# Kernel tuning notes

Hardware: AMD Instinct MI355X
Metric: run time of the kernel (lower is better)

## Reference

```python
import jax, jax.numpy as jnp
import numpy as np

B, S, D, H = 4, 1024, 768, 12
Dh = D // H
EPS = 1e-5


def _layer_norm(x, g, b):
    mu = jnp.mean(x, axis=-1, keepdims=True)
    var = jnp.var(x, axis=-1, keepdims=True)
    return (x - mu) * jax.lax.rsqrt(var + EPS) * g + b


def _mha(q_in, k_in, v_in, Wq, Wk, Wv, Wo, bias):
    # Wq/Wk/Wv: [H, D, Dh] (per-head projections, batched over heads)
    q = jnp.einsum('bsd,hdk->bhsk', q_in, Wq)
    k = jnp.einsum('btd,hdk->bhtk', k_in, Wk)
    v = jnp.einsum('btd,hdk->bhtk', v_in, Wv)
    w = jnp.einsum('bhsk,bhtk->bhst', q, k) * (Dh ** -0.5)
    a = jax.nn.softmax(w + bias, axis=-1)  # bias: 0 / -inf additive mask
    o = jnp.einsum('bhst,bhtk->bhsk', a, v)
    o = o.transpose(0, 2, 1, 3).reshape(q_in.shape[0], q_in.shape[1], H * Dh)  # concat heads
    return o @ Wo


def setup_inputs():
    key = jax.random.key(0)
    ks = jax.random.split(key, 16)
    s = 0.02
    inp = {
        'key_enc': jax.random.normal(ks[0], (B, S, D), jnp.float32),
        'value_enc': jax.random.normal(ks[1], (B, S, D), jnp.float32),
        'x': jax.random.normal(ks[2], (B, S, D), jnp.float32),
        'src_mask': jnp.ones((B, S), jnp.int32),
        'tgt_mask': jnp.ones((B, S), jnp.int32),
        'Wq_m': jax.random.normal(ks[3], (H, D, Dh), jnp.float32) * s,
        'Wk_m': jax.random.normal(ks[4], (H, D, Dh), jnp.float32) * s,
        'Wv_m': jax.random.normal(ks[5], (H, D, Dh), jnp.float32) * s,
        'Wo_m': jax.random.normal(ks[6], (D, D), jnp.float32) * s,
        'Wq_c': jax.random.normal(ks[7], (H, D, Dh), jnp.float32) * s,
        'Wk_c': jax.random.normal(ks[8], (H, D, Dh), jnp.float32) * s,
        'Wv_c': jax.random.normal(ks[9], (H, D, Dh), jnp.float32) * s,
        'Wo_c': jax.random.normal(ks[10], (D, D), jnp.float32) * s,
        'ln1_g': jnp.ones((D,), jnp.float32), 'ln1_b': jnp.zeros((D,), jnp.float32),
        'ln2_g': jnp.ones((D,), jnp.float32), 'ln2_b': jnp.zeros((D,), jnp.float32),
        'ln3_g': jnp.ones((D,), jnp.float32), 'ln3_b': jnp.zeros((D,), jnp.float32),
        'W1': jax.random.normal(ks[11], (D, 4 * D), jnp.float32) * s,
        'b1': jnp.zeros((4 * D,), jnp.float32),
        'W2': jax.random.normal(ks[12], (4 * D, D), jnp.float32) * s,
        'b2': jnp.zeros((D,), jnp.float32),
    }
    return inp


def reference(key_enc, value_enc, x, src_mask, tgt_mask,
              Wq_m, Wk_m, Wv_m, Wo_m, Wq_c, Wk_c, Wv_c, Wo_c,
              ln1_g, ln1_b, ln2_g, ln2_b, ln3_g, ln3_b, W1, b1, W2, b2):
    neg_inf = jnp.float32(-jnp.inf)
    causal = jnp.tril(jnp.ones((S, S), bool))
    # masked self-attn: causal AND target padding mask (mask broadcasts over query rows)
    allow_m = causal[None, None, :, :] & (tgt_mask[:, None, None, :] != 0)
    bias_m = jnp.where(allow_m, jnp.float32(0.0), neg_inf)
    h = _layer_norm(x + _mha(x, x, x, Wq_m, Wk_m, Wv_m, Wo_m, bias_m), ln1_g, ln1_b)
    # cross-attn: keys from `key_enc`, values from `value_enc`, queries from decoder stream
    allow_c = (src_mask[:, None, None, :] != 0)
    bias_c = jnp.where(allow_c, jnp.float32(0.0), neg_inf)
    h = _layer_norm(h + _mha(h, key_enc, value_enc, Wq_c, Wk_c, Wv_c, Wo_c, bias_c), ln2_g, ln2_b)
    # MLP with exact (erf) GELU, as torch nn.GELU default
    mlp = jax.nn.gelu(h @ W1 + b1, approximate=False) @ W2 + b2
    return _layer_norm(h + mlp, ln3_g, ln3_b)
```

## Files before the change

### kernel.cpp

```cpp
#include <hip/hip_runtime.h>
#include <math.h>

#define BB 4
#define SS 1024
#define DD 768
#define HH 12
#define DHD 64
#define MROWS 4096
#define FF 3072
#define WPC (DD * DD)
#define NSPLITROWS 24576

typedef unsigned short u16;
typedef float f32x4 __attribute__((ext_vector_type(4)));
typedef __bf16 bf16x8 __attribute__((ext_vector_type(8)));
typedef unsigned short u16x8 __attribute__((ext_vector_type(8)));
typedef unsigned short u16x4 __attribute__((ext_vector_type(4)));

static __device__ __forceinline__ float bf2f(u16 u) {
    union { unsigned int i; float f; } c; c.i = ((unsigned int)u) << 16; return c.f;
}
static __device__ __forceinline__ u16 f2bf(float f) {
    return __builtin_bit_cast(u16, static_cast<__bf16>(f));
}
static __device__ __forceinline__ int xcd_swz(int total) {
    const int bid = (int)blockIdx.x;
    return (bid & 7) * (total >> 3) + (bid >> 3);
}

#define LDST 40

static __device__ __forceinline__ void gemm128_core(
    const u16* __restrict__ A, const u16* __restrict__ Bt,
    int K,
    const float* __restrict__ bias, int do_gelu,
    u16* __restrict__ Cbf, int ldcbf, int cboff,
    int row0, int col0, u16* As, u16* Bs)
{
    const int tid  = threadIdx.x;
    const int lane = tid & 63;
    const int w    = tid >> 6;
    const int wm = (w >> 1) * 64;
    const int wn = (w & 1) * 64;

    const int srow = tid >> 1;
    const int skc  = (tid & 1) * 16;

    const u16* Ap = A  + (size_t)(row0 + srow) * K + skc;
    const u16* Bp = Bt + (size_t)(col0 + srow) * K + skc;
    u16* AsW = &As[srow * LDST + skc];
    u16* BsW = &Bs[srow * LDST + skc];

    const int fr = lane & 15;
    const int fk = (lane >> 4) * 8;

    f32x4 acc[4][4] = {};

    u16x8 aa0, aa1, ba0, ba1;
    u16x8 ab0, ab1, bb0, bb1;
    aa0 = *(const u16x8*)(Ap);
    aa1 = *(const u16x8*)(Ap + 8);
    ba0 = *(const u16x8*)(Bp);
    ba1 = *(const u16x8*)(Bp + 8);
    ab0 = *(const u16x8*)(Ap + 32);
    ab1 = *(const u16x8*)(Ap + 40);
    bb0 = *(const u16x8*)(Bp + 32);
    bb1 = *(const u16x8*)(Bp + 40);

    for (int k0 = 0; k0 < K; k0 += 64) {
        if (k0) __syncthreads();
        *(u16x8*)(AsW)     = aa0;
        *(u16x8*)(AsW + 8) = aa1;
        *(u16x8*)(BsW)     = ba0;
        *(u16x8*)(BsW + 8) = ba1;
        __syncthreads();
        if (k0 + 64 < K) {
            aa0 = *(const u16x8*)(Ap + k0 + 64);
            aa1 = *(const u16x8*)(Ap + k0 + 72);
            ba0 = *(const u16x8*)(Bp + k0 + 64);
            ba1 = *(const u16x8*)(Bp + k0 + 72);
        }
        {
            bf16x8 af[4], bfv[4];
#pragma unroll
            for (int mi = 0; mi < 4; ++mi)
                af[mi] = __builtin_bit_cast(bf16x8,
                    *(const u16x8*)(&As[(wm + 16 * mi + fr) * LDST + fk]));
#pragma unroll
            for (int ni = 0; ni < 4; ++ni)
                bfv[ni] = __builtin_bit_cast(bf16x8,
                    *(const u16x8*)(&Bs[(wn + 16 * ni + fr) * LDST + fk]));
#pragma unroll
            for (int mi = 0; mi < 4; ++mi)
#pragma unroll
                for (int ni = 0; ni < 4; ++ni)
                    acc[mi][ni] = __builtin_amdgcn_mfma_f32_16x16x32_bf16(
                        af[mi], bfv[ni], acc[mi][ni], 0, 0, 0);
        }

        __syncthreads();
        *(u16x8*)(AsW)     = ab0;
        *(u16x8*)(AsW + 8) = ab1;
        *(u16x8*)(BsW)     = bb0;
        *(u16x8*)(BsW + 8) = bb1;
        __syncthreads();
        if (k0 + 96 < K) {
            ab0 = *(const u16x8*)(Ap + k0 + 96);
            ab1 = *(const u16x8*)(Ap + k0 + 104);
            bb0 = *(const u16x8*)(Bp + k0 + 96);
            bb1 = *(const u16x8*)(Bp + k0 + 104);
        }
        {
            bf16x8 af[4], bfv[4];
#pragma unroll
            for (int mi = 0; mi < 4; ++mi)
                af[mi] = __builtin_bit_cast(bf16x8,
                    *(const u16x8*)(&As[(wm + 16 * mi + fr) * LDST + fk]));
#pragma unroll
            for (int ni = 0; ni < 4; ++ni)
                bfv[ni] = __builtin_bit_cast(bf16x8,
                    *(const u16x8*)(&Bs[(wn + 16 * ni + fr) * LDST + fk]));
#pragma unroll
            for (int mi = 0; mi < 4; ++mi)
#pragma unroll
                for (int ni = 0; ni < 4; ++ni)
                    acc[mi][ni] = __builtin_amdgcn_mfma_f32_16x16x32_bf16(
                        af[mi], bfv[ni], acc[mi][ni], 0, 0, 0);
        }
    }

    const int orow0 = row0 + wm + (lane >> 4) * 4;
    const int ocol0 = col0 + wn + fr;
#pragma unroll
    for (int mi = 0; mi < 4; ++mi) {
#pragma unroll
        for (int ni = 0; ni < 4; ++ni) {
            const int col = ocol0 + ni * 16;
            const float bv = bias ? bias[col] : 0.0f;
#pragma unroll
            for (int r = 0; r < 4; ++r) {
                const int row = orow0 + mi * 16 + r;
                float v = acc[mi][ni][r] + bv;
                if (do_gelu) v = 0.5f * v * (1.0f + erff(v * 0.70710678118654752f));
                Cbf[(size_t)row * ldcbf + cboff + col] = f2bf(v);
            }
        }
    }
}

__global__ __launch_bounds__(256) void gemm128_mlp1(
    const u16* __restrict__ A, const u16* __restrict__ Bt,
    const float* __restrict__ bias, u16* __restrict__ Cbf)
{
    __shared__ u16 As[128 * LDST];
    __shared__ u16 Bs[128 * LDST];
    const int lid = xcd_swz(24 * 32);
    gemm128_core(A, Bt, DD, bias, 1, Cbf, FF, 0,
                 (lid / 24) * 128, (lid % 24) * 128, As, Bs);
}

__global__ __launch_bounds__(256) void gemm128_proj(
    const u16* __restrict__ BFx, const u16* __restrict__ BFK,
    const u16* __restrict__ BFV, const u16* __restrict__ Wm6,
    u16* __restrict__ QKV, u16* __restrict__ KVc)
{
    __shared__ u16 As[128 * LDST];
    __shared__ u16 Bs[128 * LDST];
    const int fid = xcd_swz(960);
    const u16* A; const u16* B; u16* C; int ldc, coff, row0, col0;
    if (fid < 576) {
        A = BFx; B = Wm6; C = QKV; ldc = 3 * DD; coff = 0;
        row0 = (fid / 18) * 128; col0 = (fid % 18) * 128;
    } else if (fid < 768) {
        const int l = fid - 576;
        A = BFK; B = Wm6 + 4 * WPC; C = KVc; ldc = 2 * DD; coff = 0;
        row0 = (l / 6) * 128; col0 = (l % 6) * 128;
    } else {
        const int l = fid - 768;
        A = BFV; B = Wm6 + 5 * WPC; C = KVc; ldc = 2 * DD; coff = DD;
        row0 = (l / 6) * 128; col0 = (l % 6) * 128;
    }
    gemm128_core(A, B, DD, nullptr, 0, C, ldc, coff, row0, col0, As, Bs);
}

static __device__ __forceinline__ void gemm64_core(
    const u16* __restrict__ A, const u16* __restrict__ Bt,
    int N, int Kstride, int Klen,
    const float* __restrict__ bias,
    const float* __restrict__ residf, const u16* __restrict__ residb,
    u16* __restrict__ Cbf, int ldcbf, int cboff,
    int row0, int col0, u16* As, u16* Bs)
{
    const int tid  = threadIdx.x;
    const int lane = tid & 63;
    const int w    = tid >> 6;
    const int wm = (w >> 1) * 32;
    const int wn = (w & 1) * 64;

    const int arow = tid >> 2;
    const int akc  = (tid & 3) * 8;
    const int brow = tid >> 1;
    const int bkc  = (tid & 1) * 16;

    const u16* Ap = A  + (size_t)(row0 + arow) * Kstride + akc;
    const u16* Bp = Bt + (size_t)(col0 + brow) * Kstride + bkc;
    u16* AsW = &As[arow * LDST + akc];
    u16* BsW = &Bs[brow * LDST + bkc];

    const int fr = lane & 15;
    const int fk = (lane >> 4) * 8;

    f32x4 acc[2][4] = {};

    u16x8 a0, b00, b01, a1, b10, b11;
    a0  = *(const u16x8*)(Ap);
    b00 = *(const u16x8*)(Bp);
    b01 = *(const u16x8*)(Bp + 8);
    a1  = *(const u16x8*)(Ap + 32);
    b10 = *(const u16x8*)(Bp + 32);
    b11 = *(const u16x8*)(Bp + 40);

    for (int k0 = 0; k0 < Klen; k0 += 64) {
        if (k0) __syncthreads();
        *(u16x8*)AsW       = a0;
        *(u16x8*)BsW       = b00;
        *(u16x8*)(BsW + 8) = b01;
        __syncthreads();
        if (k0 + 64 < Klen) {
            a0  = *(const u16x8*)(Ap + k0 + 64);
            b00 = *(const u16x8*)(Bp + k0 + 64);
            b01 = *(const u16x8*)(Bp + k0 + 72);
        }
        {
            bf16x8 af[2], bfv[4];
#pragma unroll
            for (int mi = 0; mi < 2; ++mi)
                af[mi] = __builtin_bit_cast(bf16x8,
                    *(const u16x8*)(&As[(wm + 16 * mi + fr) * LDST + fk]));
#pragma unroll
            for (int ni = 0; ni < 4; ++ni)
                bfv[ni] = __builtin_bit_cast(bf16x8,
                    *(const u16x8*)(&Bs[(wn + 16 * ni + fr) * LDST + fk]));
#pragma unroll
            for (int mi = 0; mi < 2; ++mi)
#pragma unroll
                for (int ni = 0; ni < 4; ++ni)
                    acc[mi][ni] = __builtin_amdgcn_mfma_f32_16x16x32_bf16(
                        af[mi], bfv[ni], acc[mi][ni], 0, 0, 0);
        }

        __syncthreads();
        *(u16x8*)AsW       = a1;
        *(u16x8*)BsW       = b10;
        *(u16x8*)(BsW + 8) = b11;
        __syncthreads();
        if (k0 + 96 < Klen) {
            a1  = *(const u16x8*)(Ap + k0 + 96);
            b10 = *(const u16x8*)(Bp + k0 + 96);
            b11 = *(const u16x8*)(Bp + k0 + 104);
        }
        {
            bf16x8 af[2], bfv[4];
#pragma unroll
            for (int mi = 0; mi < 2; ++mi)
                af[mi] = __builtin_bit_cast(bf16x8,
                    *(const u16x8*)(&As[(wm + 16 * mi + fr) * LDST + fk]));
#pragma unroll
            for (int ni = 0; ni < 4; ++ni)
                bfv[ni] = __builtin_bit_cast(bf16x8,
                    *(const u16x8*)(&Bs[(wn + 16 * ni + fr) * LDST + fk]));
#pragma unroll
            for (int mi = 0; mi < 2; ++mi)
#pragma unroll
                for (int ni = 0; ni < 4; ++ni)
                    acc[mi][ni] = __builtin_amdgcn_mfma_f32_16x16x32_bf16(
                        af[mi], bfv[ni], acc[mi][ni], 0, 0, 0);
        }
    }

    const int orow0 = row0 + wm + (lane >> 4) * 4;
    const int ocol0 = col0 + wn + fr;
#pragma unroll
    for (int mi = 0; mi < 2; ++mi) {
#pragma unroll
        for (int ni = 0; ni < 4; ++ni) {
            const int col = ocol0 + ni * 16;
            const float bv = bias ? bias[col] : 0.0f;
#pragma unroll
            for (int r = 0; r < 4; ++r) {
                const int row = orow0 + mi * 16 + r;
                float v = acc[mi][ni][r] + bv;
                if (residf) v += residf[(size_t)row * N + col];
                if (residb) v += bf2f(residb[(size_t)row * N + col]);
                Cbf[(size_t)row * ldcbf + cboff + col] = f2bf(v);
            }
        }
    }
}

__global__ __launch_bounds__(256) void gemm64(
    const u16* __restrict__ A, const u16* __restrict__ Bt, int K,
    const float* __restrict__ residf, const u16* __restrict__ residb,
    u16* __restrict__ Cbf, int ldcbf)
{
    __shared__ u16 As[64 * LDST];
    __shared__ u16 Bs[128 * LDST];
    const int lid = xcd_swz(6 * 64);
    gemm64_core(A, Bt, DD, K, K, nullptr, residf, residb, Cbf, ldcbf, 0,
                (lid / 6) * 64, (lid % 6) * 128, As, Bs);
}

__global__ __launch_bounds__(256) void gemm64_sk(
    const u16* __restrict__ A, const u16* __restrict__ Bt,
    u16* __restrict__ Cpair)
{
    __shared__ u16 As[64 * LDST];
    __shared__ u16 Bs[128 * LDST];
    const int lid = xcd_swz(6 * 64 * 2);
    const int x = lid % 6;
    const int rem = lid / 6;
    const int y = rem % 64;
    const int z = rem / 64;
    const int koff = z * (FF / 2);
    gemm64_core(A + koff, Bt + koff, DD, FF, FF / 2,
                nullptr, nullptr, nullptr,
                Cpair + (size_t)z * MROWS * DD, DD, 0,
                y * 64, x * 128, As, Bs);
}

static __device__ __forceinline__ void tcvt_body(
    const float* __restrict__ in, u16* __restrict__ out,
    int K, int N, int bx, int by)
{
    __shared__ float t[32][33];
    const int n0 = bx * 32, k0 = by * 32;
    const int tx = threadIdx.x & 31, ty = threadIdx.x >> 5;
#pragma unroll
    for (int j = 0; j < 4; ++j)
        t[ty + j * 8][tx] = in[(size_t)(k0 + ty + j * 8) * N + n0 + tx];
    __syncthreads();
#pragma unroll
    for (int j = 0; j < 4; ++j)
        out[(size_t)(n0 + ty + j * 8) * K + k0 + tx] = f2bf(t[tx][ty + j * 8]);
}

__global__ __launch_bounds__(256) void prep_all(
    const float* __restrict__ x, const float* __restrict__ key_enc,
    const float* __restrict__ value_enc,
    u16* __restrict__ BFx, u16* __restrict__ BFK, u16* __restrict__ BFV,
    const float* __restrict__ wq_m, const float* __restrict__ wk_m,
    const float* __restrict__ wv_m, const float* __restrict__ wq_c,
    const float* __restrict__ wk_c, const float* __restrict__ wv_c,
    u16* __restrict__ Wm6,
    const float* __restrict__ wom, const float* __restrict__ woc,
    const float* __restrict__ w1, const float* __restrict__ w2,
    u16* __restrict__ womt, u16* __restrict__ woct,
    u16* __restrict__ w1t, u16* __restrict__ w2t)
{
    const int fid = (int)blockIdx.x;
    const int tid = threadIdx.x;
    if (fid < 9216) {
        const int z = fid / 3072;
        const float* s = (z == 0) ? x : (z == 1) ? key_enc : value_enc;
        u16* d = (z == 0) ? BFx : (z == 1) ? BFK : BFV;
        const int i = (fid % 3072) * 256 + tid;
        float4 v = ((const float4*)s)[i];
        ushort4 o;
        o.x = f2bf(v.x); o.y = f2bf(v.y); o.z = f2bf(v.z); o.w = f2bf(v.w);
        ((ushort4*)d)[i] = o;
    } else if (fid < 12672) {
        const int l = fid - 9216;
        const int z = l / 48;
        const int r = l % 48;
        const int wi = z / 12, head = z % 12;
        const float* wsel = (wi == 0) ? wq_m : (wi == 1) ? wk_m :
                            (wi == 2) ? wv_m : (wi == 3) ? wq_c :
                            (wi == 4) ? wk_c : wv_c;
        const float* ib = wsel + (size_t)head * DD * DHD;
        u16* ob = Wm6 + (size_t)wi * WPC + (size_t)head * DHD * DD;
        __shared__ float t[32][33];
        const int n0 = (r % 2) * 32, k0 = (r / 2) * 32;
        const int tx = tid & 31, ty = tid >> 5;
#pragma unroll
        for (int j = 0; j < 4; ++j)
            t[ty + j * 8][tx] = ib[(size_t)(k0 + ty + j * 8) * DHD + n0 + tx];
        __syncthreads();
#pragma unroll
        for (int j = 0; j < 4; ++j)
            ob[(size_t)(n0 + ty + j * 8) * DD + k0 + tx] = f2bf(t[tx][ty + j * 8]);
    } else {
        const int l = fid - 12672;
        if (l < 576) {
            tcvt_body(wom, womt, DD, DD, l % 24, l / 24);
        } else if (l < 1152) {
            const int m = l - 576;
            tcvt_body(woc, woct, DD, DD, m % 24, m / 24);
        } else if (l < 3456) {
            const int m = l - 1152;
            tcvt_body(w1, w1t, DD, FF, m % 96, m / 96);
        } else {
            const int m = l - 3456;
            tcvt_body(w2, w2t, FF, DD, m % 24, m / 24);
        }
    }
}

#define KAST 72
#define PAST 136
#define CSC 0.18033688011112042f

__global__ __launch_bounds__(256) void attn_cross_kernel(
    const u16* __restrict__ Q, int ldq,
    const u16* __restrict__ K, const u16* __restrict__ V, int ldkv,
    const int* __restrict__ kmask, u16* __restrict__ O)
{
    const int lid = xcd_swz(16 * BB * HH);
    const int qt = lid % 16;
    const int bh = lid / 16;
    const int b  = bh / HH;
    const int h  = bh % HH;
    const int tid  = threadIdx.x;
    const int lane = tid & 63;
    const int w    = tid >> 6;
    const int lr = lane & 15;
    const int lg = lane >> 4;

    __shared__ u16 Ks[128 * KAST];
    __shared__ u16 Ps[64 * PAST];
    __shared__ u16 Vt[64 * PAST];

    const int q0w = qt * 64 + w * 16;

    bf16x8 qf[2];
    {
        const u16* qp = Q + (size_t)(b * SS + q0w + lr) * ldq + h * DHD + lg * 8;
        qf[0] = __builtin_bit_cast(bf16x8, *(const u16x8*)(qp));
        qf[1] = __builtin_bit_cast(bf16x8, *(const u16x8*)(qp + 32));
    }

    const int sr  = tid >> 1;
    const int scb = (tid & 1) * 32;
    const int vk  = tid >> 1;
    const int vdb = (tid & 1) * 32;
    const int k6  = vk & 63;
    const int vcol = ((vk >> 6) << 6) | ((k6 & 15) << 2) | (k6 >> 4);

    f32x4 acc[4] = {};
    float lsum[4] = {0.0f, 0.0f, 0.0f, 0.0f};

    u16x8 kr0, kr1, kr2, kr3, vr0, vr1, vr2, vr3;
    {
        const u16* kp = K + (size_t)(b * SS + sr) * ldkv + h * DHD + scb;
        kr0 = *(const u16x8*)(kp);
        kr1 = *(const u16x8*)(kp + 8);
        kr2 = *(const u16x8*)(kp + 16);
        kr3 = *(const u16x8*)(kp + 24);
        const u16* vp = V + (size_t)(b * SS + vk) * ldkv + h * DHD + vdb;
        vr0 = *(const u16x8*)(vp);
        vr1 = *(const u16x8*)(vp + 8);
        vr2 = *(const u16x8*)(vp + 16);
        vr3 = *(const u16x8*)(vp + 24);
    }

    for (int kt = 0; kt < 8; ++kt) {
        const int kcol0 = kt * 128;
        if (kt) __syncthreads();

        *(u16x8*)(&Ks[sr * KAST + scb])      = kr0;
        *(u16x8*)(&Ks[sr * KAST + scb + 8])  = kr1;
        *(u16x8*)(&Ks[sr * KAST + scb + 16]) = kr2;
        *(u16x8*)(&Ks[sr * KAST + scb + 24]) = kr3;
#pragma unroll
        for (int j = 0; j < 8; ++j) Vt[(vdb + j) * PAST + vcol]      = vr0[j];
#pragma unroll
        for (int j = 0; j < 8; ++j) Vt[(vdb + 8 + j) * PAST + vcol]  = vr1[j];
#pragma unroll
        for (int j = 0; j < 8; ++j) Vt[(vdb + 16 + j) * PAST + vcol] = vr2[j];
#pragma unroll
        for (int j = 0; j < 8; ++j) Vt[(vdb + 24 + j) * PAST + vcol] = vr3[j];
        __syncthreads();

        if (kt + 1 < 8) {
            const int kn = kcol0 + 128;
            const u16* kp = K + (size_t)(b * SS + kn + sr) * ldkv + h * DHD + scb;
            kr0 = *(const u16x8*)(kp);
            kr1 = *(const u16x8*)(kp + 8);
            kr2 = *(const u16x8*)(kp + 16);
            kr3 = *(const u16x8*)(kp + 24);
            const u16* vp = V + (size_t)(b * SS + kn + vk) * ldkv + h * DHD + vdb;
            vr0 = *(const u16x8*)(vp);
            vr1 = *(const u16x8*)(vp + 8);
            vr2 = *(const u16x8*)(vp + 16);
            vr3 = *(const u16x8*)(vp + 24);
        }

        f32x4 s[8] = {};
#pragma unroll
        for (int fi = 0; fi < 8; ++fi) {
            bf16x8 kf0 = __builtin_bit_cast(bf16x8, *(const u16x8*)(&Ks[(fi * 16 + lr) * KAST + lg * 8]));
            bf16x8 kf1 = __builtin_bit_cast(bf16x8, *(const u16x8*)(&Ks[(fi * 16 + lr) * KAST + 32 + lg * 8]));
            s[fi] = __builtin_amdgcn_mfma_f32_16x16x32_bf16(qf[0], kf0, s[fi], 0, 0, 0);
            s[fi] = __builtin_amdgcn_mfma_f32_16x16x32_bf16(qf[1], kf1, s[fi], 0, 0, 0);
        }

        float biasf[8];
#pragma unroll
        for (int fi = 0; fi < 8; ++fi)
            biasf[fi] = kmask[b * SS + kcol0 + fi * 16 + lr] ? 0.0f : -INFINITY;

#pragma unroll
        for (int r = 0; r < 4; ++r) {
            const int prow = (w * 16 + lg * 4 + r) * PAST;
            u16x4 pk0, pk1;
            float rs = 0.0f;
#pragma unroll
            for (int fi = 0; fi < 8; ++fi) {
                const float v = fmaf(s[fi][r], CSC, biasf[fi]);
                const float pv = exp2f(v);
                if (fi < 4) pk0[fi] = f2bf(pv); else pk1[fi - 4] = f2bf(pv);
                rs += pv;
            }
            lsum[r] += rs;
            *(u16x4*)(&Ps[prow + lr * 4])      = pk0;
            *(u16x4*)(&Ps[prow + 64 + lr * 4]) = pk1;
        }

#pragma unroll
        for (int kk = 0; kk < 4; ++kk) {
            bf16x8 pf = __builtin_bit_cast(bf16x8, *(const u16x8*)(&Ps[(w * 16 + lr) * PAST + kk * 32 + lg * 8]));
#pragma unroll
            for (int di = 0; di < 4; ++di) {
                bf16x8 vf = __builtin_bit_cast(bf16x8, *(const u16x8*)(&Vt[(di * 16 + lr) * PAST + kk * 32 + lg * 8]));
                acc[di] = __builtin_amdgcn_mfma_f32_16x16x32_bf16(pf, vf, acc[di], 0, 0, 0);
            }
        }
    }

#pragma unroll
    for (int r = 0; r < 4; ++r) {
        float l = lsum[r];
        l += __shfl_xor(l, 1);
        l += __shfl_xor(l, 2);
        l += __shfl_xor(l, 4);
        l += __shfl_xor(l, 8);
        const float inv = (l > 0.0f) ? (1.0f / l) : 0.0f;
        const size_t orow = (size_t)(b * SS + q0w + lg * 4 + r) * DD + h * DHD;
#pragma unroll
        for (int di = 0; di < 4; ++di)
            O[orow + di * 16 + lr] = f2bf(acc[di][r] * inv);
    }
}

__global__ __launch_bounds__(256) void attn_self_kernel(
    const u16* __restrict__ Q, int ldq,
    const u16* __restrict__ K, const u16* __restrict__ V, int ldkv,
    const int* __restrict__ kmask, u16* __restrict__ O,
    u16* __restrict__ ACCP, float* __restrict__ LP)
{
    const int lid = xcd_swz(1152);
    int bh, qt, sp, split;
    if (lid < 768) {
        bh = lid / 16;
        const int t = lid % 16;
        qt = 8 + (t >> 1);
        sp = t & 1;
        split = 1;
    } else {
        const int l = lid - 768;
        bh = l / 8;
        qt = l % 8;
        sp = 0;
        split = 0;
    }
    const int b  = bh / HH;
    const int h  = bh % HH;
    const int tid  = threadIdx.x;
    const int lane = tid & 63;
    const int w    = tid >> 6;
    const int lr = lane & 15;
    const int lg = lane >> 4;

    __shared__ u16 Ks[128 * KAST];
    __shared__ u16 Ps[64 * PAST];
    __shared__ u16 Vt[64 * PAST];

    const int q0w = qt * 64 + w * 16;

    bf16x8 qf[2];
    {
        const u16* qp = Q + (size_t)(b * SS + q0w + lr) * ldq + h * DHD + lg * 8;
        qf[0] = __builtin_bit_cast(bf16x8, *(const u16x8*)(qp));
        qf[1] = __builtin_bit_cast(bf16x8, *(const u16x8*)(qp + 32));
    }

    const int sr  = tid >> 1;
    const int scb = (tid & 1) * 32;
    const int vk  = tid >> 1;
    const int vdb = (tid & 1) * 32;
    const int k6  = vk & 63;
    const int vcol = ((vk >> 6) << 6) | ((k6 & 15) << 2) | (k6 >> 4);

    f32x4 acc[4] = {};
    float lsum[4] = {0.0f, 0.0f, 0.0f, 0.0f};

    const int nktF = (qt + 2) >> 1;
    const int h2   = (nktF + 1) >> 1;
    const int ktBeg = split ? (sp ? h2 : 0) : 0;
    const int ktEnd = split ? (sp ? nktF : h2) : nktF;

    u16x8 kr0, kr1, kr2, kr3, vr0, vr1, vr2, vr3;
    {
        const int kn = ktBeg * 128;
        const u16* kp = K + (size_t)(b * SS + kn + sr) * ldkv + h * DHD + scb;
        kr0 = *(const u16x8*)(kp);
        kr1 = *(const u16x8*)(kp + 8);
        kr2 = *(const u16x8*)(kp + 16);
        kr3 = *(const u16x8*)(kp + 24);
        const u16* vp = V + (size_t)(b * SS + kn + vk) * ldkv + h * DHD + vdb;
        vr0 = *(const u16x8*)(vp);
        vr1 = *(const u16x8*)(vp + 8);
        vr2 = *(const u16x8*)(vp + 16);
        vr3 = *(const u16x8*)(vp + 24);
    }

    for (int kt = ktBeg; kt < ktEnd; ++kt) {
        const int kcol0 = kt * 128;
        if (kt != ktBeg) __syncthreads();

        *(u16x8*)(&Ks[sr * KAST + scb])      = kr0;
        *(u16x8*)(&Ks[sr * KAST + scb + 8])  = kr1;
        *(u16x8*)(&Ks[sr * KAST + scb + 16]) = kr2;
        *(u16x8*)(&Ks[sr * KAST + scb + 24]) = kr3;
#pragma unroll
        for (int j = 0; j < 8; ++j) Vt[(vdb + j) * PAST + vcol]      = vr0[j];
#pragma unroll
        for (int j = 0; j < 8; ++j) Vt[(vdb + 8 + j) * PAST + vcol]  = vr1[j];
#pragma unroll
        for (int j = 0; j < 8; ++j) Vt[(vdb + 16 + j) * PAST + vcol] = vr2[j];
#pragma unroll
        for (int j = 0; j < 8; ++j) Vt[(vdb + 24 + j) * PAST + vcol] = vr3[j];
        __syncthreads();

        if (kt + 1 < ktEnd) {
            const int kn = kcol0 + 128;
            const u16* kp = K + (size_t)(b * SS + kn + sr) * ldkv + h * DHD + scb;
            kr0 = *(const u16x8*)(kp);
            kr1 = *(const u16x8*)(kp + 8);
            kr2 = *(const u16x8*)(kp + 16);
            kr3 = *(const u16x8*)(kp + 24);
            const u16* vp = V + (size_t)(b * SS + kn + vk) * ldkv + h * DHD + vdb;
            vr0 = *(const u16x8*)(vp);
            vr1 = *(const u16x8*)(vp + 8);
            vr2 = *(const u16x8*)(vp + 16);
            vr3 = *(const u16x8*)(vp + 24);
        }

        f32x4 s[8] = {};
#pragma unroll
        for (int fi = 0; fi < 8; ++fi) {
            bf16x8 kf0 = __builtin_bit_cast(bf16x8, *(const u16x8*)(&Ks[(fi * 16 + lr) * KAST + lg * 8]));
            bf16x8 kf1 = __builtin_bit_cast(bf16x8, *(const u16x8*)(&Ks[(fi * 16 + lr) * KAST + 32 + lg * 8]));
            s[fi] = __builtin_amdgcn_mfma_f32_16x16x32_bf16(qf[0], kf0, s[fi], 0, 0, 0);
            s[fi] = __builtin_amdgcn_mfma_f32_16x16x32_bf16(qf[1], kf1, s[fi], 0, 0, 0);
        }

        float biasf[8];
#pragma unroll
        for (int fi = 0; fi < 8; ++fi)
            biasf[fi] = kmask[b * SS + kcol0 + fi * 16 + lr] ? 0.0f : -INFINITY;
        const bool diag = (kt == nktF - 1);

#pragma unroll
        for (int r = 0; r < 4; ++r) {
            const int qrow = q0w + lg * 4 + r;
            const int prow = (w * 16 + lg * 4 + r) * PAST;
            u16x4 pk0, pk1;
            float rs = 0.0f;
#pragma unroll
            for (int fi = 0; fi < 8; ++fi) {
                float v = fmaf(s[fi][r], CSC, biasf[fi]);
                if (diag) {
                    const int key = kcol0 + fi * 16 + lr;
                    v = (key <= qrow) ? v : -INFINITY;
                }
                const float pv = exp2f(v);
                if (fi < 4) pk0[fi] = f2bf(pv); else pk1[fi - 4] = f2bf(pv);
                rs += pv;
            }
            lsum[r] += rs;
            *(u16x4*)(&Ps[prow + lr * 4])      = pk0;
            *(u16x4*)(&Ps[prow + 64 + lr * 4]) = pk1;
        }

#pragma unroll
        for (int kk = 0; kk < 4; ++kk) {
            bf16x8 pf = __builtin_bit_cast(bf16x8, *(const u16x8*)(&Ps[(w * 16 + lr) * PAST + kk * 32 + lg * 8]));
#pragma unroll
            for (int di = 0; di < 4; ++di) {
                bf16x8 vf = __builtin_bit_cast(bf16x8, *(const u16x8*)(&Vt[(di * 16 + lr) * PAST + kk * 32 + lg * 8]));
                acc[di] = __builtin_amdgcn_mfma_f32_16x16x32_bf16(pf, vf, acc[di], 0, 0, 0);
            }
        }
    }

#pragma unroll
    for (int r = 0; r < 4; ++r) {
        float l = lsum[r];
        l += __shfl_xor(l, 1);
        l += __shfl_xor(l, 2);
        l += __shfl_xor(l, 4);
        l += __shfl_xor(l, 8);
        if (!split) {
            const float inv = (l > 0.0f) ? (1.0f / l) : 0.0f;
            const size_t orow = (size_t)(b * SS + q0w + lg * 4 + r) * DD + h * DHD;
#pragma unroll
            for (int di = 0; di < 4; ++di)
                O[orow + di * 16 + lr] = f2bf(acc[di][r] * inv);
        } else {
            const int R = bh * 512 + (qt - 8) * 64 + w * 16 + lg * 4 + r;
            u16* ap = ACCP + ((size_t)sp * NSPLITROWS + R) * 64;
#pragma unroll
            for (int di = 0; di < 4; ++di)
                ap[di * 16 + lr] = f2bf(acc[di][r]);
            if (lr == 0)
                LP[sp * NSPLITROWS + R] = l;
        }
    }
}

__global__ __launch_bounds__(256) void attn_merge_kernel(
    const u16* __restrict__ ACCP, const float* __restrict__ LP,
    u16* __restrict__ O)
{
    const int gid = (int)blockIdx.x * 256 + threadIdx.x;
    const int R  = gid >> 3;
    const int d0 = (gid & 7) * 8;
    const float l0 = LP[R];
    const float l1 = LP[NSPLITROWS + R];
    const float den = l0 + l1;
    const float inv = (den > 0.0f) ? (1.0f / den) : 0.0f;
    u16x8 a0 = *(const u16x8*)(ACCP + (size_t)R * 64 + d0);
    u16x8 a1 = *(const u16x8*)(ACCP + ((size_t)NSPLITROWS + R) * 64 + d0);
    u16x8 o;
#pragma unroll
    for (int j = 0; j < 8; ++j)
        o[j] = f2bf((bf2f(a0[j]) + bf2f(a1[j])) * inv);
    const int bh = R >> 9;
    const int r  = R & 511;
    const int b  = bh / HH;
    const int h  = bh % HH;
    const size_t orow = (size_t)(b * SS + 512 + r) * DD + h * DHD;
    *(u16x8*)(O + orow + d0) = o;
}

__global__ __launch_bounds__(256) void ln_bf_kernel(
    const u16* __restrict__ X, const float* __restrict__ gma,
    const float* __restrict__ bta, u16* __restrict__ Ybf)
{
    const int row = blockIdx.x;
    const int tid = threadIdx.x;
    const u16* x = X + (size_t)row * DD;

    const float v0 = bf2f(x[tid]);
    const float v1 = bf2f(x[tid + 256]);
    const float v2 = bf2f(x[tid + 512]);

    __shared__ float sd[256];
    sd[tid] = v0 + v1 + v2;
    __syncthreads();
    for (int off = 128; off > 0; off >>= 1) {
        if (tid < off) sd[tid] += sd[tid + off];
        __syncthreads();
    }
    const float mean = sd[0] * (1.0f / 768.0f);
    __syncthreads();

    const float q0 = v0 - mean, q1 = v1 - mean, q2 = v2 - mean;
    sd[tid] = q0 * q0 + q1 * q1 + q2 * q2;
    __syncthreads();
    for (int off = 128; off > 0; off >>= 1) {
        if (tid < off) sd[tid] += sd[tid + off];
        __syncthreads();
    }
    const float var = sd[0] * (1.0f / 768.0f);
    const float inv = rsqrtf(var + 1e-5f);

    u16* yb = Ybf + (size_t)row * DD;
    yb[tid]       = f2bf(q0 * inv * gma[tid]       + bta[tid]);
    yb[tid + 256] = f2bf(q1 * inv * gma[tid + 256] + bta[tid + 256]);
    yb[tid + 512] = f2bf(q2 * inv * gma[tid + 512] + bta[tid + 512]);
}

__global__ __launch_bounds__(256) void ln_red_kernel(
    const u16* __restrict__ P0, const u16* __restrict__ P1,
    const float* __restrict__ bias, const u16* __restrict__ resid,
    const float* __restrict__ gma, const float* __restrict__ bta,
    float* __restrict__ Y)
{
    const int row = blockIdx.x;
    const int tid = threadIdx.x;
    const size_t base = (size_t)row * DD;

    float v[3];
#pragma unroll
    for (int j = 0; j < 3; ++j) {
        const int i = tid + j * 256;
        v[j] = bf2f(P0[base + i]) + bf2f(P1[base + i]) + bias[i] + bf2f(resid[base + i]);
    }

    __shared__ float sd[256];
    sd[tid] = v[0] + v[1] + v[2];
    __syncthreads();
    for (int off = 128; off > 0; off >>= 1) {
        if (tid < off) sd[tid] += sd[tid + off];
        __syncthreads();
    }
    const float mean = sd[0] * (1.0f / 768.0f);
    __syncthreads();

    float q[3];
#pragma unroll
    for (int j = 0; j < 3; ++j) q[j] = v[j] - mean;
    sd[tid] = q[0] * q[0] + q[1] * q[1] + q[2] * q[2];
    __syncthreads();
    for (int off = 128; off > 0; off >>= 1) {
        if (tid < off) sd[tid] += sd[tid + off];
        __syncthreads();
    }
    const float var = sd[0] * (1.0f / 768.0f);
    const float inv = rsqrtf(var + 1e-5f);

    float* y = Y + base;
#pragma unroll
    for (int j = 0; j < 3; ++j) {
        const int i = tid + j * 256;
        y[i] = q[j] * inv * gma[i] + bta[i];
    }
}

extern "C" void kernel_launch(void* const* d_in, const int* in_sizes, int n_in,
                              void* d_out, int out_size, void* d_ws, size_t ws_size,
                              hipStream_t stream)
{
    (void)in_sizes; (void)n_in; (void)out_size; (void)ws_size;

    const float* key_enc   = (const float*)d_in[0];
    const float* value_enc = (const float*)d_in[1];
    const float* x         = (const float*)d_in[2];
    const int*   src_mask  = (const int*)d_in[3];
    const int*   tgt_mask  = (const int*)d_in[4];
    const float* Wq_m = (const float*)d_in[5];
    const float* Wk_m = (const float*)d_in[6];
    const float* Wv_m = (const float*)d_in[7];
    const float* Wo_m = (const float*)d_in[8];
    const float* Wq_c = (const float*)d_in[9];
    const float* Wk_c = (const float*)d_in[10];
    const float* Wv_c = (const float*)d_in[11];
    const float* Wo_c = (const float*)d_in[12];
    const float* ln1_g = (const float*)d_in[13];
    const float* ln1_b = (const float*)d_in[14];
    const float* ln2_g = (const float*)d_in[15];
    const float* ln2_b = (const float*)d_in[16];
    const float* ln3_g = (const float*)d_in[17];
    const float* ln3_b = (const float*)d_in[18];
    const float* W1 = (const float*)d_in[19];
    const float* b1 = (const float*)d_in[20];
    const float* W2 = (const float*)d_in[21];
    const float* b2 = (const float*)d_in[22];

    float* out = (float*)d_out;

    const size_t ACT = (size_t)MROWS * DD;
    char* p = (char*)d_ws;
    u16* QKV  = (u16*)p;   p += 3 * ACT * 2;
    u16* BFx  = (u16*)p;   p += ACT * 2;
    u16* BFK  = (u16*)p;   p += ACT * 2;
    u16* BFV  = (u16*)p;   p += ACT * 2;
    u16* BF1a = (u16*)p;   p += ACT * 2;
    u16* BF1h = (u16*)p;   p += ACT * 2;
    u16* T2bf = (u16*)p;   p += ACT * 2;
    u16* SKKV = (u16*)p;   p += 2 * ACT * 2;
    u16* Wm6  = (u16*)p;   p += 6 * (size_t)WPC * 2;
    u16* Wom_t = (u16*)p;  p += (size_t)WPC * 2;
    u16* Woc_t = (u16*)p;  p += (size_t)WPC * 2;
    u16* W1t  = (u16*)p;   p += (size_t)DD * FF * 2;
    u16* W2t  = (u16*)p;   p += (size_t)DD * FF * 2;
    float* LP = (float*)p; p += 2 * (size_t)NSPLITROWS * 4;
    u16* MID  = QKV;
    u16* KVc  = SKKV;
    u16* SK0  = SKKV;
    u16* SK1  = SKKV + ACT;
    u16* ACCP = T2bf;

    const dim3 blk(256);

    prep_all<<<dim3(18432), blk, 0, stream>>>(
        x, key_enc, value_enc, BFx, BFK, BFV,
        Wq_m, Wk_m, Wv_m, Wq_c, Wk_c, Wv_c, Wm6,
        Wo_m, Wo_c, W1, W2, Wom_t, Woc_t, W1t, W2t);

    gemm128_proj<<<dim3(960), blk, 0, stream>>>(BFx, BFK, BFV, Wm6, QKV, KVc);

    attn_self_kernel<<<dim3(1152), blk, 0, stream>>>(
        QKV, 3 * DD, QKV + DD, QKV + 2 * DD, 3 * DD, tgt_mask, BF1a, ACCP, LP);
    attn_merge_kernel<<<dim3(768), blk, 0, stream>>>(ACCP, LP, BF1a);
    gemm64<<<dim3(384), blk, 0, stream>>>(BF1a, Wom_t, DD,
                                          x, nullptr, T2bf, DD);
    ln_bf_kernel<<<MROWS, blk, 0, stream>>>(T2bf, ln1_g, ln1_b, BF1h);

    gemm64<<<dim3(384), blk, 0, stream>>>(BF1h, Wm6 + 3 * WPC, DD,
                                          nullptr, nullptr, QKV, 3 * DD);
    attn_cross_kernel<<<dim3(768), blk, 0, stream>>>(
        QKV, 3 * DD, KVc, KVc + DD, 2 * DD, src_mask, BF1a);
    gemm64<<<dim3(384), blk, 0, stream>>>(BF1a, Woc_t, DD,
                                          nullptr, BF1h, T2bf, DD);
    ln_bf_kernel<<<MROWS, blk, 0, stream>>>(T2bf, ln2_g, ln2_b, BF1h);

    gemm128_mlp1<<<dim3(768), blk, 0, stream>>>(BF1h, W1t, b1, MID);
    gemm64_sk<<<dim3(768), blk, 0, stream>>>(MID, W2t, SKKV);
    ln_red_kernel<<<MROWS, blk, 0, stream>>>(SK0, SK1, b2, BF1h,
                                             ln3_g, ln3_b, out);
}
```

Before: 291.4 us.

## Split cross-attention over two key halves and share K/P LDS buffer

Cross-attention now launches 1536 blocks, each covering half of the key range, and writes unnormalised partial accumulators and row sums to scratch. A merge kernel combines the halves, and that kernel is generalised so both the self- and cross-attention paths use it. The K and P shared-memory tiles are merged into one buffer, with an extra barrier per tile, to cut LDS use and raise occupancy. In exchange it adds a kernel launch, scratch round-trips through global memory, and an extra bf16 rounding of the partial sums.

Result: slower. 299.0 us (+2.6%).

```diff
diff --git a/kernel.cpp b/kernel.cpp
--- a/kernel.cpp
+++ b/kernel.cpp
@@ -9,7 +9,8 @@
 #define MROWS 4096
 #define FF 3072
 #define WPC (DD * DD)
-#define NSPLITROWS 24576
+#define NSELFROWS 24576
+#define NCROSSROWS 49152
 
 typedef unsigned short u16;
 typedef float f32x4 __attribute__((ext_vector_type(4)));
@@ -412,11 +413,14 @@
 __global__ __launch_bounds__(256) void attn_cross_kernel(
     const u16* __restrict__ Q, int ldq,
     const u16* __restrict__ K, const u16* __restrict__ V, int ldkv,
-    const int* __restrict__ kmask, u16* __restrict__ O)
-{
-    const int lid = xcd_swz(16 * BB * HH);
-    const int qt = lid % 16;
-    const int bh = lid / 16;
+    const int* __restrict__ kmask,
+    u16* __restrict__ ACCP, float* __restrict__ LP)
+{
+    const int lid = xcd_swz(1536);
+    const int bh = lid / 32;
+    const int t  = lid % 32;
+    const int qt = t >> 1;
+    const int sp = t & 1;
     const int b  = bh / HH;
     const int h  = bh % HH;
     const int tid  = threadIdx.x;
@@ -425,8 +429,7 @@
     const int lr = lane & 15;
     const int lg = lane >> 4;
 
-    __shared__ u16 Ks[128 * KAST];
-    __shared__ u16 Ps[64 * PAST];
+    __shared__ u16 KPs[128 * KAST];
     __shared__ u16 Vt[64 * PAST];
 
     const int q0w = qt * 64 + w * 16;
@@ -448,28 +451,32 @@
     f32x4 acc[4] = {};
     float lsum[4] = {0.0f, 0.0f, 0.0f, 0.0f};
 
+    const int ktBeg = sp * 4;
+    const int ktEnd = ktBeg + 4;
+
     u16x8 kr0, kr1, kr2, kr3, vr0, vr1, vr2, vr3;
     {
-        const u16* kp = K + (size_t)(b * SS + sr) * ldkv + h * DHD + scb;
+        const int kn = ktBeg * 128;
+        const u16* kp = K + (size_t)(b * SS + kn + sr) * ldkv + h * DHD + scb;
         kr0 = *(const u16x8*)(kp);
         kr1 = *(const u16x8*)(kp + 8);
         kr2 = *(const u16x8*)(kp + 16);
         kr3 = *(const u16x8*)(kp + 24);
-        const u16* vp = V + (size_t)(b * SS + vk) * ldkv + h * DHD + vdb;
+        const u16* vp = V + (size_t)(b * SS + kn + vk) * ldkv + h * DHD + vdb;
         vr0 = *(const u16x8*)(vp);
         vr1 = *(const u16x8*)(vp + 8);
         vr2 = *(const u16x8*)(vp + 16);
         vr3 = *(const u16x8*)(vp + 24);
     }
 
-    for (int kt = 0; kt < 8; ++kt) {
+    for (int kt = ktBeg; kt < ktEnd; ++kt) {
         const int kcol0 = kt * 128;
-        if (kt) __syncthreads();
-
-        *(u16x8*)(&Ks[sr * KAST + scb])      = kr0;
-        *(u16x8*)(&Ks[sr * KAST + scb + 8])  = kr1;
-        *(u16x8*)(&Ks[sr * KAST + scb + 16]) = kr2;
-        *(u16x8*)(&Ks[sr * KAST + scb + 24]) = kr3;
+        if (kt != ktBeg) __syncthreads();
+
+        *(u16x8*)(&KPs[sr * KAST + scb])      = kr0;
+        *(u16x8*)(&KPs[sr * KAST + scb + 8])  = kr1;
+        *(u16x8*)(&KPs[sr * KAST + scb + 16]) = kr2;
+        *(u16x8*)(&KPs[sr * KAST + scb + 24]) = kr3;
 #pragma unroll
         for (int j = 0; j < 8; ++j) Vt[(vdb + j) * PAST + vcol]      = vr0[j];
 #pragma unroll
@@ -480,7 +487,7 @@
         for (int j = 0; j < 8; ++j) Vt[(vdb + 24 + j) * PAST + vcol] = vr3[j];
         __syncthreads();
 
-        if (kt + 1 < 8) {
+        if (kt + 1 < ktEnd) {
             const int kn = kcol0 + 128;
             const u16* kp = K + (size_t)(b * SS + kn + sr) * ldkv + h * DHD + scb;
             kr0 = *(const u16x8*)(kp);
@@ -497,11 +504,12 @@
         f32x4 s[8] = {};
 #pragma unroll
         for (int fi = 0; fi < 8; ++fi) {
-            bf16x8 kf0 = __builtin_bit_cast(bf16x8, *(const u16x8*)(&Ks[(fi * 16 + lr) * KAST + lg * 8]));
-            bf16x8 kf1 = __builtin_bit_cast(bf16x8, *(const u16x8*)(&Ks[(fi * 16 + lr) * KAST + 32 + lg * 8]));
+            bf16x8 kf0 = __builtin_bit_cast(bf16x8, *(const u16x8*)(&KPs[(fi * 16 + lr) * KAST + lg * 8]));
+            bf16x8 kf1 = __builtin_bit_cast(bf16x8, *(const u16x8*)(&KPs[(fi * 16 + lr) * KAST + 32 + lg * 8]));
             s[fi] = __builtin_amdgcn_mfma_f32_16x16x32_bf16(qf[0], kf0, s[fi], 0, 0, 0);
             s[fi] = __builtin_amdgcn_mfma_f32_16x16x32_bf16(qf[1], kf1, s[fi], 0, 0, 0);
         }
+        __syncthreads();
 
         float biasf[8];
 #pragma unroll
@@ -521,13 +529,13 @@
                 rs += pv;
             }
             lsum[r] += rs;
-            *(u16x4*)(&Ps[prow + lr * 4])      = pk0;
-            *(u16x4*)(&Ps[prow + 64 + lr * 4]) = pk1;
+            *(u16x4*)(&KPs[prow + lr * 4])      = pk0;
+            *(u16x4*)(&KPs[prow + 64 + lr * 4]) = pk1;
         }
 
 #pragma unroll
         for (int kk = 0; kk < 4; ++kk) {
-            bf16x8 pf = __builtin_bit_cast(bf16x8, *(const u16x8*)(&Ps[(w * 16 + lr) * PAST + kk * 32 + lg * 8]));
+            bf16x8 pf = __builtin_bit_cast(bf16x8, *(const u16x8*)(&KPs[(w * 16 + lr) * PAST + kk * 32 + lg * 8]));
 #pragma unroll
             for (int di = 0; di < 4; ++di) {
                 bf16x8 vf = __builtin_bit_cast(bf16x8, *(const u16x8*)(&Vt[(di * 16 + lr) * PAST + kk * 32 + lg * 8]));
@@ -543,11 +551,13 @@
         l += __shfl_xor(l, 2);
         l += __shfl_xor(l, 4);
         l += __shfl_xor(l, 8);
-        const float inv = (l > 0.0f) ? (1.0f / l) : 0.0f;
-        const size_t orow = (size_t)(b * SS + q0w + lg * 4 + r) * DD + h * DHD;
+        const int R = bh * 1024 + qt * 64 + w * 16 + lg * 4 + r;
+        u16* ap = ACCP + ((size_t)sp * NCROSSROWS + R) * 64;
 #pragma unroll
         for (int di = 0; di < 4; ++di)
-            O[orow + di * 16 + lr] = f2bf(acc[di][r] * inv);
+            ap[di * 16 + lr] = f2bf(acc[di][r]);
+        if (lr == 0)
+            LP[sp * NCROSSROWS + R] = l;
     }
 }
 
@@ -580,8 +590,7 @@
     const int lr = lane & 15;
     const int lg = lane >> 4;
 
-    __shared__ u16 Ks[128 * KAST];
-    __shared__ u16 Ps[64 * PAST];
+    __shared__ u16 KPs[128 * KAST];
     __shared__ u16 Vt[64 * PAST];
 
     const int q0w = qt * 64 + w * 16;
@@ -627,10 +636,10 @@
         const int kcol0 = kt * 128;
         if (kt != ktBeg) __syncthreads();
 
-        *(u16x8*)(&Ks[sr * KAST + scb])      = kr0;
-        *(u16x8*)(&Ks[sr * KAST + scb + 8])  = kr1;
-        *(u16x8*)(&Ks[sr * KAST + scb + 16]) = kr2;
-        *(u16x8*)(&Ks[sr * KAST + scb + 24]) = kr3;
+        *(u16x8*)(&KPs[sr * KAST + scb])      = kr0;
+        *(u16x8*)(&KPs[sr * KAST + scb + 8])  = kr1;
+        *(u16x8*)(&KPs[sr * KAST + scb + 16]) = kr2;
+        *(u16x8*)(&KPs[sr * KAST + scb + 24]) = kr3;
 #pragma unroll
         for (int j = 0; j < 8; ++j) Vt[(vdb + j) * PAST + vcol]      = vr0[j];
 #pragma unroll
@@ -658,11 +667,12 @@
         f32x4 s[8] = {};
 #pragma unroll
         for (int fi = 0; fi < 8; ++fi) {
-            bf16x8 kf0 = __builtin_bit_cast(bf16x8, *(const u16x8*)(&Ks[(fi * 16 + lr) * KAST + lg * 8]));
-            bf16x8 kf1 = __builtin_bit_cast(bf16x8, *(const u16x8*)(&Ks[(fi * 16 + lr) * KAST + 32 + lg * 8]));
+            bf16x8 kf0 = __builtin_bit_cast(bf16x8, *(const u16x8*)(&KPs[(fi * 16 + lr) * KAST + lg * 8]));
+            bf16x8 kf1 = __builtin_bit_cast(bf16x8, *(const u16x8*)(&KPs[(fi * 16 + lr) * KAST + 32 + lg * 8]));
             s[fi] = __builtin_amdgcn_mfma_f32_16x16x32_bf16(qf[0], kf0, s[fi], 0, 0, 0);
             s[fi] = __builtin_amdgcn_mfma_f32_16x16x32_bf16(qf[1], kf1, s[fi], 0, 0, 0);
         }
+        __syncthreads();
 
         float biasf[8];
 #pragma unroll
@@ -688,13 +698,13 @@
                 rs += pv;
             }
             lsum[r] += rs;
-            *(u16x4*)(&Ps[prow + lr * 4])      = pk0;
-            *(u16x4*)(&Ps[prow + 64 + lr * 4]) = pk1;
+            *(u16x4*)(&KPs[prow + lr * 4])      = pk0;
+            *(u16x4*)(&KPs[prow + 64 + lr * 4]) = pk1;
         }
 
 #pragma unroll
         for (int kk = 0; kk < 4; ++kk) {
-            bf16x8 pf = __builtin_bit_cast(bf16x8, *(const u16x8*)(&Ps[(w * 16 + lr) * PAST + kk * 32 + lg * 8]));
+            bf16x8 pf = __builtin_bit_cast(bf16x8, *(const u16x8*)(&KPs[(w * 16 + lr) * PAST + kk * 32 + lg * 8]));
 #pragma unroll
             for (int di = 0; di < 4; ++di) {
                 bf16x8 vf = __builtin_bit_cast(bf16x8, *(const u16x8*)(&Vt[(di * 16 + lr) * PAST + kk * 32 + lg * 8]));
@@ -718,38 +728,38 @@
                 O[orow + di * 16 + lr] = f2bf(acc[di][r] * inv);
         } else {
             const int R = bh * 512 + (qt - 8) * 64 + w * 16 + lg * 4 + r;
-            u16* ap = ACCP + ((size_t)sp * NSPLITROWS + R) * 64;
+            u16* ap = ACCP + ((size_t)sp * NSELFROWS + R) * 64;
 #pragma unroll
             for (int di = 0; di < 4; ++di)
                 ap[di * 16 + lr] = f2bf(acc[di][r]);
             if (lr == 0)
-                LP[sp * NSPLITROWS + R] = l;
+                LP[sp * NSELFROWS + R] = l;
         }
     }
 }
 
 __global__ __launch_bounds__(256) void attn_merge_kernel(
     const u16* __restrict__ ACCP, const float* __restrict__ LP,
-    u16* __restrict__ O)
+    u16* __restrict__ O, int NR, int rowsPerBh, int baseRow)
 {
     const int gid = (int)blockIdx.x * 256 + threadIdx.x;
     const int R  = gid >> 3;
     const int d0 = (gid & 7) * 8;
     const float l0 = LP[R];
-    const float l1 = LP[NSPLITROWS + R];
+    const float l1 = LP[NR + R];
     const float den = l0 + l1;
     const float inv = (den > 0.0f) ? (1.0f / den) : 0.0f;
     u16x8 a0 = *(const u16x8*)(ACCP + (size_t)R * 64 + d0);
-    u16x8 a1 = *(const u16x8*)(ACCP + ((size_t)NSPLITROWS + R) * 64 + d0);
+    u16x8 a1 = *(const u16x8*)(ACCP + ((size_t)NR + R) * 64 + d0);
     u16x8 o;
 #pragma unroll
     for (int j = 0; j < 8; ++j)
         o[j] = f2bf((bf2f(a0[j]) + bf2f(a1[j])) * inv);
-    const int bh = R >> 9;
-    const int r  = R & 511;
+    const int bh = R / rowsPerBh;
+    const int rl = R % rowsPerBh;
     const int b  = bh / HH;
     const int h  = bh % HH;
-    const size_t orow = (size_t)(b * SS + 512 + r) * DD + h * DHD;
+    const size_t orow = (size_t)(b * SS + baseRow + rl) * DD + h * DHD;
     *(u16x8*)(O + orow + d0) = o;
 }
 
@@ -885,12 +895,12 @@
     u16* Woc_t = (u16*)p;  p += (size_t)WPC * 2;
     u16* W1t  = (u16*)p;   p += (size_t)DD * FF * 2;
     u16* W2t  = (u16*)p;   p += (size_t)DD * FF * 2;
-    float* LP = (float*)p; p += 2 * (size_t)NSPLITROWS * 4;
     u16* MID  = QKV;
     u16* KVc  = SKKV;
     u16* SK0  = SKKV;
     u16* SK1  = SKKV + ACT;
-    u16* ACCP = T2bf;
+    u16*   ACCP = BFx;
+    float* LP   = (float*)BFV;
 
     const dim3 blk(256);
 
@@ -903,15 +913,18 @@
 
     attn_self_kernel<<<dim3(1152), blk, 0, stream>>>(
         QKV, 3 * DD, QKV + DD, QKV + 2 * DD, 3 * DD, tgt_mask, BF1a, ACCP, LP);
-    attn_merge_kernel<<<dim3(768), blk, 0, stream>>>(ACCP, LP, BF1a);
+    attn_merge_kernel<<<dim3(NSELFROWS * 8 / 256), blk, 0, stream>>>(
+        ACCP, LP, BF1a, NSELFROWS, 512, 512);
     gemm64<<<dim3(384), blk, 0, stream>>>(BF1a, Wom_t, DD,
                                           x, nullptr, T2bf, DD);
     ln_bf_kernel<<<MROWS, blk, 0, stream>>>(T2bf, ln1_g, ln1_b, BF1h);
 
     gemm64<<<dim3(384), blk, 0, stream>>>(BF1h, Wm6 + 3 * WPC, DD,
                                           nullptr, nullptr, QKV, 3 * DD);
-    attn_cross_kernel<<<dim3(768), blk, 0, stream>>>(
-        QKV, 3 * DD, KVc, KVc + DD, 2 * DD, src_mask, BF1a);
+    attn_cross_kernel<<<dim3(1536), blk, 0, stream>>>(
+        QKV, 3 * DD, KVc, KVc + DD, 2 * DD, src_mask, ACCP, LP);
+    attn_merge_kernel<<<dim3(NCROSSROWS * 8 / 256), blk, 0, stream>>>(
+        ACCP, LP, BF1a, NCROSSROWS, 1024, 0);
     gemm64<<<dim3(384), blk, 0, stream>>>(BF1a, Woc_t, DD,
                                           nullptr, BF1h, T2bf, DD);
     ln_bf_kernel<<<MROWS, blk, 0, stream>>>(T2bf, ln2_g, ln2_b, BF1h);
```
